# Kernel tuning notes

Measured on AMD Instinct MI355X. Metric: run time of the kernel, lower is better.

The kernel has to match this reference:

```python
import jax, jax.numpy as jnp
import numpy as np

# ---- static configuration mirroring data_hub metadata ----
N_NODES = 10000      # atoms in the cell
N_EDGES = 250000     # (a, b, periodic-image) pairs
N_RBF = 10           # radial basis functions
MUL = 16             # multiplicity per irrep (mul_in == mul_out)
L_LIST = [0, 1, 2]   # l_in_list == l_out_list
LF_MAX = 4           # max filter angular momentum (max_l_in analog)

def _paths():
    ps = []
    for io, lo in enumerate(L_LIST):
        for ii, li in enumerate(L_LIST):
            for lf in range(abs(lo - li), min(lo + li, LF_MAX) + 1):
                ps.append((io, ii, lf))
    return ps

PATHS = _paths()  # 19 (l_out, l_in, l_f) CG paths
FEAT_OFF = np.cumsum([0] + [MUL * (2 * l + 1) for l in L_LIST]).tolist()
FEAT_IN = FEAT_OFF[-1]   # 144; output layout is identical
CG_TOTAL = int(sum((2 * L_LIST[io] + 1) * (2 * L_LIST[ii] + 1) * (2 * lf + 1) for io, ii, lf in PATHS))  # 1225
P_TOTAL = len(PATHS) * MUL * MUL  # 4864 radial weight columns
Y_DIM = (LF_MAX + 1) ** 2  # 25


def setup_inputs() -> dict:
    key = jax.random.key(0)
    ks = jax.random.split(key, 8)
    features = jax.random.normal(ks[0], (N_NODES, FEAT_IN), jnp.float32)
    R = jax.random.normal(ks[1], (N_RBF, P_TOTAL), jnp.float32) * 0.1
    Ys = jax.random.normal(ks[2], (N_EDGES, Y_DIM), jnp.float32)
    radii = jax.random.uniform(ks[3], (N_EDGES, N_RBF), jnp.float32)
    cg_flat = jax.random.normal(ks[4], (CG_TOTAL,), jnp.float32)
    n_norm = jax.random.uniform(ks[5], (N_NODES,), jnp.float32)
    map_a = jax.random.randint(ks[6], (N_EDGES,), 0, N_NODES, jnp.int32)
    map_b = jax.random.randint(ks[7], (N_EDGES,), 0, N_NODES, jnp.int32)
    return {"features": features, "R": R, "Ys": Ys, "radii": radii,
            "cg_flat": cg_flat, "n_norm": n_norm,
            "map_ab_p_to_a": map_a, "map_ab_p_to_b": map_b}


def reference(features, R, Ys, radii, cg_flat, n_norm, map_ab_p_to_a, map_ab_p_to_b):
    """SE(3) tensor-product periodic convolution:
    per (a,b,image) pair, gather source features, contract with CG blocks,
    spherical harmonics, and radial weights (radii @ R) per (l_out,l_in,l_f)
    path, then scatter-add messages onto destination nodes and scale by n_norm.
    """
    E = radii.shape[0]
    F_b = features[map_ab_p_to_b]  # [E, FEAT_IN] gather per periodic-image pair
    out_blocks = [jnp.zeros((E, MUL * (2 * l + 1)), features.dtype) for l in L_LIST]
    cg_off = 0
    for p_idx, (io, ii, lf) in enumerate(PATHS):
        lo, li = L_LIST[io], L_LIST[ii]
        do, di, df = 2 * lo + 1, 2 * li + 1, 2 * lf + 1
        cg = cg_flat[cg_off:cg_off + do * di * df].reshape(do, di, df)
        cg_off += do * di * df
        Fp = F_b[:, FEAT_OFF[ii]:FEAT_OFF[ii] + MUL * di].reshape(E, MUL, di)
        Yp = Ys[:, lf * lf:lf * lf + df]  # [E, 2lf+1]
        # per-edge radial mixing weights for this path: [E, mul_out, mul_in]
        Wp = (radii @ R[:, p_idx * MUL * MUL:(p_idx + 1) * MUL * MUL]).reshape(E, MUL, MUL)
        norm = np.float32(1.0 / np.sqrt(df))  # norm_coef per path
        # CG tensor product of input irrep with spherical harmonics -> output irrep
        tmp = jnp.einsum('evi,ef,oif->evo', Fp, Yp, cg) * norm  # [E, mul_in, 2lo+1]
        out_blocks[io] = out_blocks[io] + jnp.einsum('ewv,evo->ewo', Wp, tmp).reshape(E, MUL * do)
    B = jnp.concatenate(out_blocks, axis=1)  # [E, FEAT_IN] per-pair messages
    # scatter-add over periodic images onto destination atoms (index_add_)
    F_next = jax.ops.segment_sum(B, map_ab_p_to_a, num_segments=N_NODES)
    return F_next * n_norm[:, None]
```

## Files before the change

### kernel.cpp

```cpp
#include <hip/hip_runtime.h>
#include <hip/hip_bf16.h>

#define NP   19
#define EPB  16
#define BLK  256
#define RSTRIDE 4864

#define ESA  256
#define PBSA (16*ESA)
#define ESB  160
#define PBSB (16*ESB)
#define CGS  392
#define MINBPC 4

typedef __attribute__((ext_vector_type(8))) short bf16x8;
typedef __attribute__((ext_vector_type(4))) float f32x4;

__device__ const int   d_io[NP]  = {0,0,0, 1,1,1,1,1,1,1, 2,2,2,2, 2,2,2,2,2};
__device__ const int   d_ii[NP]  = {0,1,2, 0,1,1,1,2,2,2, 0,1,1,1, 2,2,2,2,2};
__device__ const int   d_lf[NP]  = {0,1,2, 1,0,1,2,1,2,3, 2,1,2,3, 0,1,2,3,4};
__device__ const int   d_cgb[NP] = {0,1,10, 35,44,53,80,125,170,245, 350,375,420,495, 600,625,700,825,1000};
__device__ const int   d_cgyb[NP] = {380,280,0, 381,284,296,308, 8,32,56, 384,320,340,360, 80,120,160,200,240};
__device__ const float d_nrm5[5] = {1.0f, 0.57735026918962576f, 0.44721359549995794f,
                                    0.37796447300922722f, 0.33333333333333333f};

__device__ __forceinline__ unsigned short to_bf16(float v) {
    __hip_bfloat16 h = __float2bfloat16(v);
    return *reinterpret_cast<unsigned short*>(&h);
}
__device__ __forceinline__ float bf2f(unsigned short u) {
    unsigned int x = ((unsigned int)u) << 16;
    union { unsigned int i; float f; } c; c.i = x;
    return c.f;
}

__global__ void k_rt(const float* __restrict__ R, unsigned short* __restrict__ Rt) {
    int i = blockIdx.x * blockDim.x + threadIdx.x;
    if (i >= NP * 16 * 64 * 8) return;
    const int j    = i & 7;
    const int lane = (i >> 3) & 63;
    const int t    = (i >> 9) & 15;
    const int p    = i >> 13;
    const int r    = (lane >> 4) * 8 + j;
    const int col  = p * 256 + 16 * t + (lane & 15);
    float v = (r < 10) ? R[r * RSTRIDE + col] : 0.f;
    Rt[i] = to_bf16(v);
}

__global__ __launch_bounds__(BLK, MINBPC)
void se3_msg(const float* __restrict__ F,
             const float* __restrict__ Ys, const float* __restrict__ Rad,
             const float* __restrict__ cg, const unsigned short* __restrict__ Rt,
             const int* __restrict__ Mb, const int* __restrict__ Ma,
             const int* __restrict__ eidx, const float* __restrict__ Nn,
             float* __restrict__ Out, const int nE)
{
    __shared__ __align__(16) unsigned short s_Wa[2 * PBSA];
    __shared__ __align__(16) unsigned short s_tB[2 * PBSB + 256];
    __shared__ __align__(16) unsigned short s_cgy16[EPB * CGS];
    __shared__ int   s_dest[EPB];
    __shared__ float s_nn[EPB];

    const int tid  = threadIdx.x;
    const int l    = tid & 15;
    const int eloc = tid >> 4;
    const int lane = tid & 63;
    const int wv   = tid >> 6;
    const int q    = lane >> 4;
    const int n16  = lane & 15;
    const int slot = blockIdx.x * EPB + eloc;
    const bool act = (slot < nE);
    const int  es  = act ? eidx[slot] : 0;

    if (tid < EPB) {
        const int sl = blockIdx.x * EPB + tid;
        int a = -1; float nn = 0.f;
        if (sl < nE) { a = Ma[eidx[sl]]; nn = Nn[a]; }
        s_dest[tid] = a; s_nn[tid] = nn;
    }

    float fv[9];
    {
        const int b = Mb[es];
        const float* Fb = F + (size_t)b * 144;
        fv[0] = Fb[l];
        #pragma unroll
        for (int i = 0; i < 3; ++i) fv[1 + i] = Fb[16 + l*3 + i];
        #pragma unroll
        for (int i = 0; i < 5; ++i) fv[4 + i] = Fb[64 + l*5 + i];
    }
    float y[25];
    {
        const float* yr = Ys + (size_t)es * 25;
        #pragma unroll
        for (int k = 0; k < 25; ++k) y[k] = yr[k];
    }
    bf16x8 radfrag;
    {
        const int k0 = q * 8;
        const int gslot = blockIdx.x * EPB + n16;
        const bool a = (gslot < nE);
        const int  ge = a ? eidx[gslot] : 0;
        const float* rp = Rad + (size_t)ge * 10;
        #pragma unroll
        for (int j = 0; j < 8; ++j) {
            const int k = k0 + j;
            radfrag[j] = (short)((a && k < 10) ? to_bf16(rp[k]) : (unsigned short)0);
        }
    }

    const int keyB = (eloc & 3) << 3;
    const int rowB = eloc * ESB;

    {
        #pragma unroll
        for (int n = 0; n < 10; ++n) {
            const int off = (rowB + (n << 4) + l) ^ keyB;
            s_tB[off] = 0; s_tB[PBSB + off] = 0;
        }
    }

    {
        #pragma unroll
        for (int p = 0; p < NP; ++p) {
            const int io = d_io[p], ii = d_ii[p], lf = d_lf[p];
            const int cgb = d_cgb[p], cb = d_cgyb[p];
            const int dO = 2*io + 1, dI = 2*ii + 1, dF = 2*lf + 1;
            const int nOI = dO * dI;
            const float nrm = d_nrm5[lf];
            #pragma unroll
            for (int jj = 0; jj < 2; ++jj) {
                const int j = l + 16*jj;
                if (j < nOI) {
                    const int o = j / dI, i = j - o*dI;
                    const float* cgp = cg + cgb + j*dF;
                    float s = 0.f;
                    #pragma unroll
                    for (int f = 0; f < dF; ++f) s += cgp[f] * y[lf*lf + f];
                    const int off = (dI == 1) ? o : (dI == 3) ? (o*4 + i) : (o*8 + i);
                    s_cgy16[eloc*CGS + cb + off] = to_bf16(s * nrm);
                }
            }
        }
    }
    __asm__ volatile("" ::: "memory");

    bf16x8 rf[2][4];
    {
        const unsigned short* r0 = Rt + (size_t)(4*wv)*512 + lane*8;
        #pragma unroll
        for (int tt = 0; tt < 4; ++tt) rf[0][tt] = *reinterpret_cast<const bf16x8*>(r0 + tt*512);
    }

    f32x4 D[4];
    #pragma unroll
    for (int ee = 0; ee < 4; ++ee) D[ee] = (f32x4){0.f,0.f,0.f,0.f};

    #pragma unroll
    for (int kb = 0; kb < 10; ++kb) {
        #pragma unroll
        for (int pb = 0; pb < 2; ++pb) {
            const int p = 2*kb + pb;
            if (p + 1 < NP) {
                const unsigned short* rn = Rt + (size_t)(p+1)*8192 + (size_t)(4*wv)*512 + lane*8;
                #pragma unroll
                for (int tt = 0; tt < 4; ++tt)
                    rf[pb ^ 1][tt] = *reinterpret_cast<const bf16x8*>(rn + tt*512);
            }
            if (p < NP) {
                #pragma unroll
                for (int tt = 0; tt < 4; ++tt) {
                    f32x4 d = __builtin_amdgcn_mfma_f32_16x16x32_bf16(
                                  rf[pb][tt], radfrag, (f32x4){0.f,0.f,0.f,0.f}, 0, 0, 0);
                    short4 pk;
                    pk.x = (short)to_bf16(d[0]); pk.y = (short)to_bf16(d[1]);
                    pk.z = (short)to_bf16(d[2]); pk.w = (short)to_bf16(d[3]);
                    const int w = 4*wv + tt;
                    *reinterpret_cast<short4*>(
                        &s_Wa[pb*PBSA + (((n16 << 8) + (w << 4) + (q << 2)) ^ ((n16 & 7) << 3))]) = pk;
                }

                const int io = d_io[p], ii = d_ii[p], cb = d_cgyb[p];
                const int dO = 2*io + 1;
                const int ob  = (io == 0) ? 0 : (io == 1) ? 1 : 4;

                const unsigned short* cgw = &s_cgy16[eloc*CGS + cb];
                unsigned short* tbh = &s_tB[pb*PBSB];
                if (p == 3 || p == 4)        { tbh[(rowB + l) ^ keyB] = 0; }
                else if (p == 10 || p == 11) { tbh[(rowB + 16 + l) ^ keyB] = 0;
                                               tbh[(rowB + 32 + l) ^ keyB] = 0;
                                               tbh[(rowB + 48 + l) ^ keyB] = 0; }
                if (ii == 0) {
                    #pragma unroll
                    for (int o = 0; o < dO; ++o) {
                        const float c0 = bf2f(cgw[o]);
                        tbh[(rowB + ((ob + o) << 4) + l) ^ keyB] = to_bf16(fv[0]*c0);
                    }
                } else if (ii == 1) {
                    #pragma unroll
                    for (int o = 0; o < dO; ++o) {
                        const short4 c = *reinterpret_cast<const short4*>(&cgw[o*4]);
                        tbh[(rowB + ((ob + o) << 4) + l) ^ keyB] =
                            to_bf16(fv[1]*bf2f((unsigned short)c.x)
                                  + fv[2]*bf2f((unsigned short)c.y)
                                  + fv[3]*bf2f((unsigned short)c.z));
                    }
                } else {
                    #pragma unroll
                    for (int o = 0; o < dO; ++o) {
                        const bf16x8 c = *reinterpret_cast<const bf16x8*>(&cgw[o*8]);
                        tbh[(rowB + ((ob + o) << 4) + l) ^ keyB] =
                            to_bf16(fv[4]*bf2f((unsigned short)c[0])
                                  + fv[5]*bf2f((unsigned short)c[1])
                                  + fv[6]*bf2f((unsigned short)c[2])
                                  + fv[7]*bf2f((unsigned short)c[3])
                                  + fv[8]*bf2f((unsigned short)c[4]));
                    }
                }
            } else {
                const short4 z = {0, 0, 0, 0};
                #pragma unroll
                for (int tt = 0; tt < 4; ++tt) {
                    const int w = 4*wv + tt;
                    *reinterpret_cast<short4*>(
                        &s_Wa[pb*PBSA + (((n16 << 8) + (w << 4) + (q << 2)) ^ ((n16 & 7) << 3))]) = z;
                }
            }
        }
        __syncthreads();

        {
            const int kh = q >> 1;
            const int vh = (q & 1) << 3;
            #pragma unroll
            for (int ee = 0; ee < 4; ++ee) {
                const int eK   = 4*wv + ee;
                const bf16x8 Af = *reinterpret_cast<const bf16x8*>(
                    &s_Wa[kh*PBSA + (((eK << 8) + (n16 << 4) + vh) ^ ((eK & 7) << 3))]);
                const bf16x8 Bf = *reinterpret_cast<const bf16x8*>(
                    &s_tB[kh*PBSB + ((eK*ESB + (n16 << 4) + vh) ^ ((eK & 3) << 3))]);
                D[ee] = __builtin_amdgcn_mfma_f32_16x16x32_bf16(Af, Bf, D[ee], 0, 0, 0);
            }
        }
        __syncthreads();
    }

    float* sred = reinterpret_cast<float*>(s_Wa);
    if (n16 < 9) {
        #pragma unroll
        for (int ee = 0; ee < 4; ++ee) {
            float4 v4; v4.x = D[ee][0]; v4.y = D[ee][1]; v4.z = D[ee][2]; v4.w = D[ee][3];
            *reinterpret_cast<float4*>(&sred[(4*wv + ee)*160 + n16*16 + q*4]) = v4;
        }
    }
    __syncthreads();

    if (tid < 144) {
        const int w  = tid & 15;
        const int of = tid >> 4;
        const int oidx = (of == 0) ? w : (of <= 3) ? (16 + w*3 + (of - 1)) : (64 + w*5 + (of - 4));
        const int col = of*16 + w;
        int i = 0;
        while (i < EPB) {
            const int a = s_dest[i];
            if (a < 0) { ++i; continue; }
            float s = 0.f;
            int j = i;
            do { s += sred[j*160 + col]; ++j; } while (j < EPB && s_dest[j] == a);
            atomicAdd(&Out[(size_t)a * 144 + oidx], s * s_nn[i]);
            i = j;
        }
    }
}

__global__ void k_count(const int* __restrict__ Ma, int* __restrict__ cur, int E) {
    int e = blockIdx.x * blockDim.x + threadIdx.x;
    if (e < E) atomicAdd(&cur[Ma[e]], 1);
}

__global__ void k_scan(int* __restrict__ cur, int* __restrict__ off, int N) {
    __shared__ int part[BLK];
    const int t = threadIdx.x;
    const int K = (N + BLK - 1) / BLK;
    const int i0 = t * K, i1 = min(i0 + K, N);
    int s = 0;
    for (int i = i0; i < i1; ++i) s += cur[i];
    part[t] = s;
    __syncthreads();
    if (t == 0) {
        int a = 0;
        for (int j = 0; j < BLK; ++j) { int v = part[j]; part[j] = a; a += v; }
        off[N] = a;
    }
    __syncthreads();
    int a = part[t];
    for (int i = i0; i < i1; ++i) {
        int v = cur[i];
        off[i] = a;
        cur[i] = a;
        a += v;
    }
}

__global__ void k_scatter(const int* __restrict__ Ma, int* __restrict__ cur,
                          int* __restrict__ eidx, int E) {
    int e = blockIdx.x * blockDim.x + threadIdx.x;
    if (e < E) {
        int pos = atomicAdd(&cur[Ma[e]], 1);
        eidx[pos] = e;
    }
}

extern "C" void kernel_launch(void* const* d_in, const int* in_sizes, int n_in,
                              void* d_out, int out_size, void* d_ws, size_t ws_size,
                              hipStream_t stream) {
    const float* F   = (const float*)d_in[0];
    const float* R   = (const float*)d_in[1];
    const float* Ys  = (const float*)d_in[2];
    const float* Rad = (const float*)d_in[3];
    const float* cg  = (const float*)d_in[4];
    const float* Nn  = (const float*)d_in[5];
    const int*   Ma  = (const int*)d_in[6];
    const int*   Mb  = (const int*)d_in[7];
    float* Out = (float*)d_out;

    const int nE = in_sizes[6];
    const int nN = in_sizes[5];

    int* wsI  = (int*)d_ws;
    int* cur  = wsI;
    int* off  = wsI + nN;
    int* eidx = wsI + 2*nN + 1;
    size_t rtOff = ((size_t)(2*nN + 1 + nE) + 63) & ~(size_t)63;
    unsigned short* Rt = (unsigned short*)((float*)d_ws + rtOff);

    hipMemsetAsync(cur, 0, (size_t)nN * sizeof(int), stream);
    hipMemsetAsync(Out, 0, (size_t)nN * 144 * sizeof(float), stream);
    k_count  <<<(nE + BLK - 1) / BLK, BLK, 0, stream>>>(Ma, cur, nE);
    k_scan   <<<1, BLK, 0, stream>>>(cur, off, nN);
    k_scatter<<<(nE + BLK - 1) / BLK, BLK, 0, stream>>>(Ma, cur, eidx, nE);
    k_rt     <<<(NP*16*64*8 + BLK - 1) / BLK, BLK, 0, stream>>>(R, Rt);

    se3_msg<<<(nE + EPB - 1) / EPB, BLK, 0, stream>>>(F, Ys, Rad, cg, Rt, Mb, Ma, eidx, Nn, Out, nE);
}
```

Baseline: 490.9 us.

## Process one path per stage with single LDS buffers, halving shared memory

Replaces the two-paths-per-K32-MFMA staging, which used double-size W and tB LDS buffers, with one path per iteration. Half of each MFMA K dimension is zero-padded, so the W and tB buffers shrink to a single copy. The reduction scratch moves into s_cgy16. This cuts LDS footprint, which may allow more resident blocks. In exchange it roughly doubles the number of __syncthreads barriers (19 stages instead of 10) and wastes half of each edge-contraction MFMA.

```diff
diff --git a/kernel.cpp b/kernel.cpp
--- a/kernel.cpp
+++ b/kernel.cpp
@@ -7,9 +7,9 @@
 #define RSTRIDE 4864
 
 #define ESA  256
-#define PBSA (16*ESA)
+#define WAS  (16*ESA)
 #define ESB  160
-#define PBSB (16*ESB)
+#define TBS  (16*ESB)
 #define CGS  392
 #define MINBPC 4
 
@@ -55,8 +55,8 @@
              const int* __restrict__ eidx, const float* __restrict__ Nn,
              float* __restrict__ Out, const int nE)
 {
-    __shared__ __align__(16) unsigned short s_Wa[2 * PBSA];
-    __shared__ __align__(16) unsigned short s_tB[2 * PBSB + 256];
+    __shared__ __align__(16) unsigned short s_Wa[WAS];
+    __shared__ __align__(16) unsigned short s_tB[TBS + 256];
     __shared__ __align__(16) unsigned short s_cgy16[EPB * CGS];
     __shared__ int   s_dest[EPB];
     __shared__ float s_nn[EPB];
@@ -116,7 +116,7 @@
         #pragma unroll
         for (int n = 0; n < 10; ++n) {
             const int off = (rowB + (n << 4) + l) ^ keyB;
-            s_tB[off] = 0; s_tB[PBSB + off] = 0;
+            s_tB[off] = 0;
         }
     }
 
@@ -157,95 +157,85 @@
     for (int ee = 0; ee < 4; ++ee) D[ee] = (f32x4){0.f,0.f,0.f,0.f};
 
     #pragma unroll
-    for (int kb = 0; kb < 10; ++kb) {
-        #pragma unroll
-        for (int pb = 0; pb < 2; ++pb) {
-            const int p = 2*kb + pb;
-            if (p + 1 < NP) {
-                const unsigned short* rn = Rt + (size_t)(p+1)*8192 + (size_t)(4*wv)*512 + lane*8;
-                #pragma unroll
-                for (int tt = 0; tt < 4; ++tt)
-                    rf[pb ^ 1][tt] = *reinterpret_cast<const bf16x8*>(rn + tt*512);
-            }
-            if (p < NP) {
-                #pragma unroll
-                for (int tt = 0; tt < 4; ++tt) {
-                    f32x4 d = __builtin_amdgcn_mfma_f32_16x16x32_bf16(
-                                  rf[pb][tt], radfrag, (f32x4){0.f,0.f,0.f,0.f}, 0, 0, 0);
-                    short4 pk;
-                    pk.x = (short)to_bf16(d[0]); pk.y = (short)to_bf16(d[1]);
-                    pk.z = (short)to_bf16(d[2]); pk.w = (short)to_bf16(d[3]);
-                    const int w = 4*wv + tt;
-                    *reinterpret_cast<short4*>(
-                        &s_Wa[pb*PBSA + (((n16 << 8) + (w << 4) + (q << 2)) ^ ((n16 & 7) << 3))]) = pk;
+    for (int p = 0; p < NP; ++p) {
+        if (p + 1 < NP) {
+            const unsigned short* rn = Rt + (size_t)(p+1)*8192 + (size_t)(4*wv)*512 + lane*8;
+            #pragma unroll
+            for (int tt = 0; tt < 4; ++tt)
+                rf[(p & 1) ^ 1][tt] = *reinterpret_cast<const bf16x8*>(rn + tt*512);
+        }
+
+        #pragma unroll
+        for (int tt = 0; tt < 4; ++tt) {
+            f32x4 d = __builtin_amdgcn_mfma_f32_16x16x32_bf16(
+                          rf[p & 1][tt], radfrag, (f32x4){0.f,0.f,0.f,0.f}, 0, 0, 0);
+            short4 pk;
+            pk.x = (short)to_bf16(d[0]); pk.y = (short)to_bf16(d[1]);
+            pk.z = (short)to_bf16(d[2]); pk.w = (short)to_bf16(d[3]);
+            const int w = 4*wv + tt;
+            *reinterpret_cast<short4*>(
+                &s_Wa[(((n16 << 8) + (w << 4) + (q << 2)) ^ ((n16 & 7) << 3))]) = pk;
+        }
+
+        const int io = d_io[p], ii = d_ii[p], cb = d_cgyb[p];
+        const int dO = 2*io + 1;
+        const int ob  = (io == 0) ? 0 : (io == 1) ? 1 : 4;
+
+        const unsigned short* cgw = &s_cgy16[eloc*CGS + cb];
+        unsigned short* tbh = s_tB;
+        if (p == 3)       { tbh[(rowB + l) ^ keyB] = 0; }
+        else if (p == 10) { tbh[(rowB + 16 + l) ^ keyB] = 0;
+                            tbh[(rowB + 32 + l) ^ keyB] = 0;
+                            tbh[(rowB + 48 + l) ^ keyB] = 0; }
+        if (ii == 0) {
+            #pragma unroll
+            for (int o = 0; o < dO; ++o) {
+                const float c0 = bf2f(cgw[o]);
+                tbh[(rowB + ((ob + o) << 4) + l) ^ keyB] = to_bf16(fv[0]*c0);
+            }
+        } else if (ii == 1) {
+            #pragma unroll
+            for (int o = 0; o < dO; ++o) {
+                const short4 c = *reinterpret_cast<const short4*>(&cgw[o*4]);
+                tbh[(rowB + ((ob + o) << 4) + l) ^ keyB] =
+                    to_bf16(fv[1]*bf2f((unsigned short)c.x)
+                          + fv[2]*bf2f((unsigned short)c.y)
+                          + fv[3]*bf2f((unsigned short)c.z));
+            }
+        } else {
+            #pragma unroll
+            for (int o = 0; o < dO; ++o) {
+                const bf16x8 c = *reinterpret_cast<const bf16x8*>(&cgw[o*8]);
+                tbh[(rowB + ((ob + o) << 4) + l) ^ keyB] =
+                    to_bf16(fv[4]*bf2f((unsigned short)c[0])
+                          + fv[5]*bf2f((unsigned short)c[1])
+                          + fv[6]*bf2f((unsigned short)c[2])
+                          + fv[7]*bf2f((unsigned short)c[3])
+                          + fv[8]*bf2f((unsigned short)c[4]));
+            }
+        }
+
+        __syncthreads();
+
+        {
+            const bf16x8 zero8 = {0,0,0,0,0,0,0,0};
+            #pragma unroll
+            for (int ee = 0; ee < 4; ++ee) {
+                const int eK = 4*wv + ee;
+                bf16x8 Af = zero8, Bf = zero8;
+                if (q < 2) {
+                    Af = *reinterpret_cast<const bf16x8*>(
+                        &s_Wa[(((eK << 8) + (n16 << 4) + (q << 3)) ^ ((eK & 7) << 3))]);
+                    Bf = *reinterpret_cast<const bf16x8*>(
+                        &s_tB[((eK*ESB + (n16 << 4) + (q << 3)) ^ ((eK & 3) << 3))]);
                 }
-
-                const int io = d_io[p], ii = d_ii[p], cb = d_cgyb[p];
-                const int dO = 2*io + 1;
-                const int ob  = (io == 0) ? 0 : (io == 1) ? 1 : 4;
-
-                const unsigned short* cgw = &s_cgy16[eloc*CGS + cb];
-                unsigned short* tbh = &s_tB[pb*PBSB];
-                if (p == 3 || p == 4)        { tbh[(rowB + l) ^ keyB] = 0; }
-                else if (p == 10 || p == 11) { tbh[(rowB + 16 + l) ^ keyB] = 0;
-                                               tbh[(rowB + 32 + l) ^ keyB] = 0;
-                                               tbh[(rowB + 48 + l) ^ keyB] = 0; }
-                if (ii == 0) {
-                    #pragma unroll
-                    for (int o = 0; o < dO; ++o) {
-                        const float c0 = bf2f(cgw[o]);
-                        tbh[(rowB + ((ob + o) << 4) + l) ^ keyB] = to_bf16(fv[0]*c0);
-                    }
-                } else if (ii == 1) {
-                    #pragma unroll
-                    for (int o = 0; o < dO; ++o) {
-                        const short4 c = *reinterpret_cast<const short4*>(&cgw[o*4]);
-                        tbh[(rowB + ((ob + o) << 4) + l) ^ keyB] =
-                            to_bf16(fv[1]*bf2f((unsigned short)c.x)
-                                  + fv[2]*bf2f((unsigned short)c.y)
-                                  + fv[3]*bf2f((unsigned short)c.z));
-                    }
-                } else {
-                    #pragma unroll
-                    for (int o = 0; o < dO; ++o) {
-                        const bf16x8 c = *reinterpret_cast<const bf16x8*>(&cgw[o*8]);
-                        tbh[(rowB + ((ob + o) << 4) + l) ^ keyB] =
-                            to_bf16(fv[4]*bf2f((unsigned short)c[0])
-                                  + fv[5]*bf2f((unsigned short)c[1])
-                                  + fv[6]*bf2f((unsigned short)c[2])
-                                  + fv[7]*bf2f((unsigned short)c[3])
-                                  + fv[8]*bf2f((unsigned short)c[4]));
-                    }
-                }
-            } else {
-                const short4 z = {0, 0, 0, 0};
-                #pragma unroll
-                for (int tt = 0; tt < 4; ++tt) {
-                    const int w = 4*wv + tt;
-                    *reinterpret_cast<short4*>(
-                        &s_Wa[pb*PBSA + (((n16 << 8) + (w << 4) + (q << 2)) ^ ((n16 & 7) << 3))]) = z;
-                }
+                D[ee] = __builtin_amdgcn_mfma_f32_16x16x32_bf16(Af, Bf, D[ee], 0, 0, 0);
             }
         }
         __syncthreads();
-
-        {
-            const int kh = q >> 1;
-            const int vh = (q & 1) << 3;
-            #pragma unroll
-            for (int ee = 0; ee < 4; ++ee) {
-                const int eK   = 4*wv + ee;
-                const bf16x8 Af = *reinterpret_cast<const bf16x8*>(
-                    &s_Wa[kh*PBSA + (((eK << 8) + (n16 << 4) + vh) ^ ((eK & 7) << 3))]);
-                const bf16x8 Bf = *reinterpret_cast<const bf16x8*>(
-                    &s_tB[kh*PBSB + ((eK*ESB + (n16 << 4) + vh) ^ ((eK & 3) << 3))]);
-                D[ee] = __builtin_amdgcn_mfma_f32_16x16x32_bf16(Af, Bf, D[ee], 0, 0, 0);
-            }
-        }
-        __syncthreads();
-    }
-
-    float* sred = reinterpret_cast<float*>(s_Wa);
+    }
+
+    float* sred = reinterpret_cast<float*>(s_cgy16);
     if (n16 < 9) {
         #pragma unroll
         for (int ee = 0; ee < 4; ++ee) {
```

After: 550.7 us. 12.2% more time.
